# Kernel optimization log

Measured on AMD Instinct MI355X. Metric: run time of the kernel, lower is better.

The kernel has to match this reference:

```python
import jax, jax.numpy as jnp
import numpy as np

N = 50000          # nodes
E = 800000         # edges (avg degree 16)
NFEAT = 128        # dim_touched / gcn_nfeat
NHID = 96
NCLASS = 64
EXTRA = 32         # extra MLP-only features
NHID1, NHID2 = 128, 64
NN = 70            # top-k threshold rank
EPS = 1e-5         # BatchNorm1d eps


def setup_inputs() -> dict:
    key = jax.random.key(0)
    ks = jax.random.split(key, 24)
    x = jax.random.normal(ks[0], (N, NFEAT + EXTRA + 1), jnp.float32)
    grp = jax.random.randint(ks[1], (N,), 0, 2).astype(jnp.float32)
    x = x.at[:, -1].set(grp)  # last column is the group flag (target_group == 0)
    row = jax.random.randint(ks[2], (E,), 0, N, dtype=jnp.int32)
    col = jax.random.randint(ks[3], (E,), 0, N, dtype=jnp.int32)
    val = jax.random.uniform(ks[4], (E,), jnp.float32)

    def p(k, shape):
        return (jax.random.normal(k, shape, jnp.float32) * 0.05)

    return dict(
        x=x, row=row, col=col, val=val,
        W1=p(ks[5], (NFEAT, NHID)), b1=p(ks[6], (NHID,)),
        W2=p(ks[7], (NHID, NHID)), b2=p(ks[8], (NHID,)),
        W3=p(ks[9], (NHID, NHID)), b3=p(ks[10], (NHID,)),
        W4=p(ks[11], (NHID, NHID)), b4=p(ks[12], (NHID,)),
        W5=p(ks[13], (NHID, NCLASS)), b5=p(ks[14], (NCLASS,)),
        M1w=p(ks[15], (NCLASS + EXTRA, NHID1)), M1b=p(ks[16], (NHID1,)),
        M2w=p(ks[17], (NHID1, NHID2)), M2b=p(ks[18], (NHID2,)),
        M3w=p(ks[19], (NHID2, 1)), M3b=p(ks[20], (1,)),
    )


def _bn(h):
    # fresh BatchNorm1d in training mode, affine at default init (gamma=1, beta=0)
    m = jnp.mean(h, axis=0)
    v = jnp.mean((h - m) ** 2, axis=0)  # biased variance, as used for normalization
    return (h - m) * jax.lax.rsqrt(v + EPS)


def _gc(h, row, col, val, W, b):
    # GraphConvolution: spmm(adj, h @ W) + b, adj in COO form
    s = h @ W                                            # [N, out]
    msg = val[:, None] * s[col]                          # [E, out]
    agg = jax.ops.segment_sum(msg, row, num_segments=N)  # [N, out]
    return agg + b


def reference(x, row, col, val, W1, b1, W2, b2, W3, b3, W4, b4, W5, b5,
              M1w, M1b, M2w, M2b, M3w, M3b):
    h = x[:, :NFEAT]
    h = _bn(jax.nn.relu(_gc(h, row, col, val, W1, b1)))
    h = _bn(jax.nn.relu(_gc(h, row, col, val, W2, b2)))
    h = _bn(jax.nn.relu(_gc(h, row, col, val, W3, b3)))
    h = _bn(jax.nn.relu(_gc(h, row, col, val, W4, b4)))
    h = jax.nn.relu(_gc(h, row, col, val, W5, b5))        # [N, NCLASS]

    feat = jnp.concatenate([h, x[:, NFEAT:-1]], axis=1)   # [N, NCLASS+EXTRA]
    m = jax.nn.relu(feat @ M1w + M1b)
    m = jax.nn.relu(m @ M2w + M2b)
    m = m @ M3w + M3b                                     # [N, 1]

    # mask out target_group rows with the global min
    m = jnp.where(x[:, -1:] == 0.0, jnp.min(m), m)        # [N, 1]

    # top-70 threshold: value at descending rank NN
    thresh = jax.lax.top_k(m[:, 0], NN + 1)[0][NN]
    recip = jax.lax.stop_gradient(1.0 / m)                # torch reciprocal on detach()
    mask = jnp.where(m > thresh, recip, jnp.zeros_like(m))
    return m * mask
```

## Files before the change

kernel.cpp:

```cpp
#include <hip/hip_runtime.h>
#include <cstdint>
#include <cstddef>

#define XLD 161

typedef float f4u __attribute__((ext_vector_type(4), aligned(4)));
typedef float f4a __attribute__((ext_vector_type(4)));
typedef float f3u __attribute__((ext_vector_type(3), aligned(4)));

__global__ void hist_kernel(const int* __restrict__ row, int* __restrict__ cnt, int E) {
    for (int e = blockIdx.x * blockDim.x + threadIdx.x; e < E; e += gridDim.x * blockDim.x)
        atomicAdd(&cnt[row[e]], 1);
}

__global__ __launch_bounds__(256)
void scan1_kernel(const int* __restrict__ cnt, int* __restrict__ offs,
                  int* __restrict__ bsums, int n) {
    int t = threadIdx.x;
    int gid = blockIdx.x * 256 + t;
    int v = (gid < n) ? cnt[gid] : 0;
    int x = v;
#pragma unroll
    for (int o = 1; o < 64; o <<= 1) { int y = __shfl_up(x, o); if ((t & 63) >= o) x += y; }
    __shared__ int ws[4];
    if ((t & 63) == 63) ws[t >> 6] = x;
    __syncthreads();
    int add = 0;
    for (int w = 0; w < (t >> 6); w++) add += ws[w];
    int incl = x + add;
    if (gid < n) offs[gid] = incl - v;
    if (t == 255) bsums[blockIdx.x] = incl;
}

__global__ __launch_bounds__(256)
void scan2_kernel(int* __restrict__ bsums, int nb) {
    int t = threadIdx.x;
    int v = (t < nb) ? bsums[t] : 0;
    int x = v;
#pragma unroll
    for (int o = 1; o < 64; o <<= 1) { int y = __shfl_up(x, o); if ((t & 63) >= o) x += y; }
    __shared__ int ws[4];
    if ((t & 63) == 63) ws[t >> 6] = x;
    __syncthreads();
    int add = 0;
    for (int w = 0; w < (t >> 6); w++) add += ws[w];
    if (t < nb) bsums[t] = x + add - v;
}

__global__ void scan3_kernel(int* __restrict__ offs, int* __restrict__ cursor,
                             const int* __restrict__ bsums, int n, int E) {
    int gid = blockIdx.x * 256 + threadIdx.x;
    if (gid < n) {
        int o = offs[gid] + bsums[blockIdx.x];
        offs[gid] = o;
        cursor[gid] = o;
    }
    if (gid == 0) offs[n] = E;
}

__global__ void scatter_kernel(const int* __restrict__ row, const int* __restrict__ col,
                               const float* __restrict__ val, int* __restrict__ cursor,
                               int2* __restrict__ cvA, int E) {
    for (int e = blockIdx.x * blockDim.x + threadIdx.x; e < E; e += gridDim.x * blockDim.x) {
        int r = row[e];
        int p = atomicAdd(&cursor[r], 1);
        cvA[p] = make_int2(col[e], __float_as_int(val[e]));
    }
}

template <int LC, bool WVS>
__global__ __launch_bounds__(256)
void aggP(const float* __restrict__ S, int ldS, const int* __restrict__ offs,
          const int2* __restrict__ cvA,
          float* __restrict__ Aout, float* __restrict__ vout, int n) {
    int lane = threadIdx.x & 63;
    int lg   = lane & 31;
    int grp  = threadIdx.x >> 5;
    int sh   = lane & 32;

    for (int node = blockIdx.x * 8 + grp; node < n; node += gridDim.x * 8) {
        int e0 = offs[node], e1 = offs[node + 1];
        float acc[LC];
#pragma unroll
        for (int a = 0; a < LC; a++) acc[a] = 0.f;
        float vsum = 0.f;

        for (int e = e0; e < e1; e += 32) {
            int   idx = e + lg;
            int2  cv = (idx < e1) ? cvA[idx] : make_int2(0, 0);
            int   ce = cv.x;
            float ve = __int_as_float(cv.y);
            int   cnt = min(32, e1 - e);
#pragma unroll 8
            for (int j = 0; j < cnt; j++) {
                int   c = __shfl(ce, sh + j);
                float v = __shfl(ve, sh + j);
                const float* srow = S + (size_t)c * ldS + LC * lg;
                if (LC == 3) {
                    f3u g = *(const f3u*)srow;
                    acc[0] = fmaf(v, g[0], acc[0]);
                    acc[1] = fmaf(v, g[1], acc[1]);
                    acc[2] = fmaf(v, g[2], acc[2]);
                } else {
                    f4u g = *(const f4u*)srow;
                    acc[0] = fmaf(v, g[0], acc[0]);
                    acc[1] = fmaf(v, g[1], acc[1]);
                    acc[2] = fmaf(v, g[2], acc[2]);
                    acc[3] = fmaf(v, g[3], acc[3]);
                }
                vsum += v;
            }
        }

        float* orow = Aout + (size_t)node * (32 * LC) + LC * lg;
        if (LC == 3) {
            f3u o; o[0] = acc[0]; o[1] = acc[1]; o[2] = acc[2];
            *(f3u*)orow = o;
        } else {
            f4u o; o[0] = acc[0]; o[1] = acc[1]; o[2] = acc[2]; o[3] = acc[3];
            *(f4u*)orow = o;
        }
        if (WVS && lg == 0) vout[node] = vsum;
    }
}

__global__ __launch_bounds__(256)
void aggB(const float* __restrict__ S, const int* __restrict__ offs,
          const int2* __restrict__ cvA, const float* __restrict__ bias,
          float* __restrict__ Hout, float* __restrict__ vout,
          float* __restrict__ bsum, float* __restrict__ bsumsq, int n) {
    __shared__ float sS[96], sQ[96];
    int t = threadIdx.x;
    if (t < 96) { sS[t] = 0.f; sQ[t] = 0.f; }
    __syncthreads();
    int lane = t & 63, lg = lane & 31, grp = t >> 5, sh = lane & 32;
    float bb[3];
    bb[0] = bias[3 * lg]; bb[1] = bias[3 * lg + 1]; bb[2] = bias[3 * lg + 2];
    float ps[3] = {0.f, 0.f, 0.f}, pq[3] = {0.f, 0.f, 0.f};

    for (int node = blockIdx.x * 8 + grp; node < n; node += gridDim.x * 8) {
        int e0 = offs[node], e1 = offs[node + 1];
        float acc[3] = {0.f, 0.f, 0.f};
        float vsum = 0.f;
        for (int e = e0; e < e1; e += 32) {
            int   idx = e + lg;
            int2  cv = (idx < e1) ? cvA[idx] : make_int2(0, 0);
            int   ce = cv.x;
            float ve = __int_as_float(cv.y);
            int   cnt = min(32, e1 - e);
#pragma unroll 8
            for (int j = 0; j < cnt; j++) {
                int   c = __shfl(ce, sh + j);
                float v = __shfl(ve, sh + j);
                const float* srow = S + (size_t)c * 96 + 3 * lg;
                f3u g = *(const f3u*)srow;
                acc[0] = fmaf(v, g[0], acc[0]);
                acc[1] = fmaf(v, g[1], acc[1]);
                acc[2] = fmaf(v, g[2], acc[2]);
                vsum += v;
            }
        }
        float* orow = Hout + (size_t)node * 96 + 3 * lg;
        f3u o;
#pragma unroll
        for (int a = 0; a < 3; a++) {
            float v = fmaxf(acc[a] + bb[a], 0.f);
            o[a] = v;
            ps[a] += v; pq[a] += v * v;
        }
        *(f3u*)orow = o;
        if (lg == 0) vout[node] = vsum;
    }
#pragma unroll
    for (int a = 0; a < 3; a++) {
        atomicAdd(&sS[3 * lg + a], ps[a]);
        atomicAdd(&sQ[3 * lg + a], pq[a]);
    }
    __syncthreads();
    if (t < 96) {
        atomicAdd(&bsum[t], sS[t]);
        atomicAdd(&bsumsq[t], sQ[t]);
    }
}

template <int CT>
__device__ inline void ldw(const float* p, float* wv) {
    if constexpr (CT == 4) { *(f4a*)wv = *(const f4a*)p; }
    else if constexpr (CT == 6) { *(f3u*)wv = *(const f3u*)p; *(f3u*)(wv + 3) = *(const f3u*)(p + 3); }
    else { *(f4a*)wv = *(const f4a*)p; *(f4a*)(wv + 4) = *(const f4a*)(p + 4); }
}

template <int K, int C, bool DOBN, bool HASCB, bool LIN = false>
__global__ __launch_bounds__(256)
void gemmF(const float* __restrict__ A1, int ld1, int split,
           const float* __restrict__ A2, int ld2,
           const float* __restrict__ W, const float* __restrict__ bias,
           const float* __restrict__ cbv, const float* __restrict__ vsum,
           float* __restrict__ Out, float* __restrict__ bsum,
           float* __restrict__ bsumsq, int n) {
    constexpr int CT = C / 16;
    __shared__ float Wc[16 * C];
    __shared__ float At[16][68];
    __shared__ float redS[DOBN ? C : 1];
    __shared__ float redQ[DOBN ? C : 1];

    int t  = threadIdx.x;
    int tc = t & 15, tr = t >> 4;
    int row0 = blockIdx.x * 64;

    if (DOBN && t < C) { redS[t] = 0.f; redQ[t] = 0.f; }

    int srow = t >> 2;
    int gr = row0 + srow; if (gr >= n) gr = n - 1;
    int kh = (t & 3) * 4;

    float acc[4][CT];
#pragma unroll
    for (int i = 0; i < 4; i++)
#pragma unroll
        for (int c = 0; c < CT; c++) acc[i][c] = 0.f;

    for (int kb = 0; kb < K; kb += 16) {
        __syncthreads();
        for (int i = t * 4; i < 16 * C; i += 1024)
            *(f4a*)&Wc[i] = *(const f4u*)&W[(size_t)kb * C + i];
        {
            int kg = kb + kh;
            const float* src = (kg < split) ? (A1 + (size_t)gr * ld1 + kg)
                                            : (A2 + (size_t)gr * ld2 + (kg - split));
            f4u v = *(const f4u*)src;
#pragma unroll
            for (int e = 0; e < 4; e++) At[kh + e][srow] = v[e];
        }
        __syncthreads();
#pragma unroll
        for (int kk = 0; kk < 16; kk++) {
            f4a av = *(const f4a*)&At[kk][tr * 4];
            float wv[CT];
            ldw<CT>(&Wc[kk * C + tc * CT], wv);
#pragma unroll
            for (int i = 0; i < 4; i++)
#pragma unroll
                for (int c = 0; c < CT; c++) acc[i][c] = fmaf(av[i], wv[c], acc[i][c]);
        }
    }

    float bb[CT], cc[CT];
#pragma unroll
    for (int c = 0; c < CT; c++) {
        bb[c] = LIN ? 0.f : bias[tc * CT + c];
        cc[c] = HASCB ? cbv[tc * CT + c] : 0.f;
    }
    float ps[CT], pq[CT];
#pragma unroll
    for (int c = 0; c < CT; c++) { ps[c] = 0.f; pq[c] = 0.f; }

#pragma unroll
    for (int i = 0; i < 4; i++) {
        int r = row0 + tr * 4 + i;
        if (r < n) {
            float vs = HASCB ? vsum[r] : 0.f;
            float* o = Out + (size_t)r * C + tc * CT;
#pragma unroll
            for (int c = 0; c < CT; c++) {
                float v = acc[i][c] + vs * cc[c] + bb[c];
                if (!LIN) v = fmaxf(v, 0.f);
                o[c] = v;
                if (DOBN) { ps[c] += v; pq[c] += v * v; }
            }
        }
    }
    if (DOBN) {
#pragma unroll
        for (int c = 0; c < CT; c++) {
            ps[c] += __shfl_xor(ps[c], 16);
            ps[c] += __shfl_xor(ps[c], 32);
            pq[c] += __shfl_xor(pq[c], 16);
            pq[c] += __shfl_xor(pq[c], 32);
        }
        if ((t & 48) == 0) {
#pragma unroll
            for (int c = 0; c < CT; c++) {
                atomicAdd(&redS[tc * CT + c], ps[c]);
                atomicAdd(&redQ[tc * CT + c], pq[c]);
            }
        }
        __syncthreads();
        if (t < C) {
            atomicAdd(&bsum[t], redS[t]);
            atomicAdd(&bsumsq[t], redQ[t]);
        }
    }
}

template <int C>
__global__ __launch_bounds__(256)
void fold_kernel(const float* __restrict__ W, float* __restrict__ bsum,
                 float* __restrict__ bsumsq, float* __restrict__ Wf,
                 float* __restrict__ cb, int N) {
    __shared__ float mean[96], inv[96];
    int t = threadIdx.x;
    float rn = 1.0f / (float)N;
    if (t < 96) {
        float mu  = bsum[t] * rn;
        float var = bsumsq[t] * rn - mu * mu;
        mean[t] = mu;
        inv[t]  = rsqrtf(var + 1e-5f);
        bsum[t] = 0.f;
        bsumsq[t] = 0.f;
    }
    __syncthreads();
    for (int i = t; i < 96 * C; i += 256) {
        int k = i / C;
        Wf[i] = inv[k] * W[i];
    }
    if (t < C) {
        float s = 0.f;
        for (int k = 0; k < 96; k++) s += mean[k] * inv[k] * W[k * C + t];
        cb[t] = -s;
    }
}

__global__ __launch_bounds__(256)
void dot_min_kernel(const float* __restrict__ A, const float* __restrict__ M3w,
                    const float* __restrict__ M3b, float* __restrict__ m,
                    unsigned* __restrict__ gmin, int n) {
    int lane = threadIdx.x & 63;
    int wv   = threadIdx.x >> 6;
    float w  = M3w[lane];
    float b  = M3b[0];
    float lmin = 3.4e38f;
    int nw = gridDim.x * 4;
    for (int r = blockIdx.x * 4 + wv; r < n; r += nw) {
        float v = A[(size_t)r * 64 + lane] * w;
#pragma unroll
        for (int o = 32; o; o >>= 1) v += __shfl_down(v, o);
        if (lane == 0) {
            float mv = v + b;
            m[r] = mv;
            lmin = fminf(lmin, mv);
        }
    }
#pragma unroll
    for (int o = 32; o; o >>= 1) lmin = fminf(lmin, __shfl_down(lmin, o));
    __shared__ float sm[4];
    if (lane == 0) sm[wv] = lmin;
    __syncthreads();
    if (threadIdx.x == 0) {
        float mn = fminf(fminf(sm[0], sm[1]), fminf(sm[2], sm[3]));
        unsigned u = __float_as_uint(mn);
        unsigned key = (u >> 31) ? ~u : (u | 0x80000000u);
        atomicMin(gmin, key);
    }
}

__global__ void where_kernel(const float* __restrict__ x, float* __restrict__ m,
                             const unsigned* __restrict__ gmin, int n) {
    int i = blockIdx.x * blockDim.x + threadIdx.x;
    if (i < n) {
        unsigned k = *gmin;
        unsigned u = (k >> 31) ? (k ^ 0x80000000u) : ~k;
        float g = __uint_as_float(u);
        if (x[(size_t)i * XLD + 160] == 0.0f) m[i] = g;
    }
}

__device__ inline unsigned fkey(float f) {
    unsigned u = __float_as_uint(f);
    return (u >> 31) ? ~u : (u | 0x80000000u);
}

__global__ __launch_bounds__(256)
void sel_hist8(const float* __restrict__ m, unsigned* __restrict__ h0, int n) {
    __shared__ unsigned lh[256];
    int t = threadIdx.x;
    lh[t] = 0u;
    __syncthreads();
    for (int i = blockIdx.x * 256 + t; i < n; i += gridDim.x * 256)
        atomicAdd(&lh[fkey(m[i]) >> 24], 1u);
    __syncthreads();
    if (lh[t]) atomicAdd(&h0[t], lh[t]);
}

__global__ __launch_bounds__(256)
void sel_pick8(const unsigned* __restrict__ h, const unsigned* __restrict__ kres,
               int kconst, unsigned* __restrict__ outb, unsigned* __restrict__ outk) {
    int t = threadIdx.x;
    int bin = 255 - t;
    unsigned k = kres ? *kres : (unsigned)kconst;
    unsigned c = h[bin];
    unsigned x = c;
#pragma unroll
    for (int o = 1; o < 64; o <<= 1) { unsigned y = __shfl_up(x, o); if ((t & 63) >= o) x += y; }
    __shared__ unsigned ws[4];
    if ((t & 63) == 63) ws[t >> 6] = x;
    __syncthreads();
    unsigned add = 0;
    for (int w = 0; w < (t >> 6); w++) add += ws[w];
    unsigned incl = x + add, excl = incl - c;
    if (excl < k && k <= incl) { *outb = (unsigned)bin; *outk = k - excl; }
}

__global__ __launch_bounds__(256)
void sel_hist8b(const float* __restrict__ m, const unsigned* __restrict__ pick,
                unsigned* __restrict__ h1, int n) {
    __shared__ unsigned lh[256];
    int t = threadIdx.x;
    lh[t] = 0u;
    __syncthreads();
    unsigned b0 = pick[0];
    for (int i = blockIdx.x * 256 + t; i < n; i += gridDim.x * 256) {
        unsigned key = fkey(m[i]);
        if ((key >> 24) == b0) atomicAdd(&lh[(key >> 16) & 255u], 1u);
    }
    __syncthreads();
    if (lh[t]) atomicAdd(&h1[t], lh[t]);
}

__global__ void sel_collect(const float* __restrict__ m, const unsigned* __restrict__ pick,
                            unsigned* __restrict__ sbuf, unsigned* __restrict__ scnt, int n) {
    unsigned pfx = (pick[0] << 8) | pick[2];
    for (int i = blockIdx.x * blockDim.x + threadIdx.x; i < n; i += gridDim.x * blockDim.x) {
        unsigned key = fkey(m[i]);
        if ((key >> 16) == pfx) sbuf[atomicAdd(scnt, 1u)] = key;
    }
}

__global__ __launch_bounds__(1024)
void sel_final(const unsigned* __restrict__ sbuf, const unsigned* __restrict__ scnt,
               const unsigned* __restrict__ pick, float* __restrict__ thresh) {
    __shared__ unsigned hist[256];
    __shared__ unsigned spfx;
    __shared__ int skk;
    int t = threadIdx.x;
    int ns = (int)*scnt;
    if (t == 0) { spfx = ((pick[0] << 8) | pick[2]) << 16; skk = (int)pick[3]; }
    __syncthreads();
    for (int pass = 0; pass < 2; ++pass) {
        if (t < 256) hist[t] = 0u;
        __syncthreads();
        int shift = 8 - 8 * pass;
        unsigned pfxmask = (pass == 0) ? 0xFFFF0000u : 0xFFFFFF00u;
        unsigned pfx = spfx;
        for (int i = t; i < ns; i += 1024) {
            unsigned key = sbuf[i];
            if ((key & pfxmask) == pfx) atomicAdd(&hist[(key >> shift) & 255u], 1u);
        }
        __syncthreads();
        if (t == 0) {
            int cum = 0, kk = skk, chosen = 0;
            for (int b = 255; b >= 0; b--) {
                cum += (int)hist[b];
                if (cum >= kk) { chosen = b; kk -= (cum - (int)hist[b]); break; }
            }
            spfx = pfx | ((unsigned)chosen << shift);
            skk = kk;
        }
        __syncthreads();
    }
    if (t == 0) {
        unsigned key = spfx;
        unsigned u = (key >> 31) ? (key ^ 0x80000000u) : ~key;
        *thresh = __uint_as_float(u);
    }
}

__global__ void mask_kernel(const float* __restrict__ m, const float* __restrict__ thresh,
                            float* __restrict__ out, int n) {
    int i = blockIdx.x * blockDim.x + threadIdx.x;
    if (i < n) {
        float t = *thresh, v = m[i];
        out[i] = (v > t) ? v * (1.0f / v) : 0.0f;
    }
}

extern "C" void kernel_launch(void* const* d_in, const int* in_sizes, int n_in,
                              void* d_out, int out_size, void* d_ws, size_t ws_size,
                              hipStream_t stream) {
    const float* x   = (const float*)d_in[0];
    const int*   row = (const int*)d_in[1];
    const int*   col = (const int*)d_in[2];
    const float* val = (const float*)d_in[3];
    const float* W1  = (const float*)d_in[4];
    const float* b1  = (const float*)d_in[5];
    const float* W2  = (const float*)d_in[6];
    const float* b2  = (const float*)d_in[7];
    const float* W3  = (const float*)d_in[8];
    const float* b3  = (const float*)d_in[9];
    const float* W4  = (const float*)d_in[10];
    const float* b4  = (const float*)d_in[11];
    const float* W5  = (const float*)d_in[12];
    const float* b5  = (const float*)d_in[13];
    const float* M1w = (const float*)d_in[14];
    const float* M1b = (const float*)d_in[15];
    const float* M2w = (const float*)d_in[16];
    const float* M2b = (const float*)d_in[17];
    const float* M3w = (const float*)d_in[18];
    const float* M3b = (const float*)d_in[19];

    const int n = in_sizes[0] / XLD;
    const int E = in_sizes[1];

    char* ws = (char*)d_ws;
    size_t off = 0;
    auto carve = [&](size_t bytes) -> void* {
        void* p = ws + off;
        off = (off + bytes + 255) & ~(size_t)255;
        return p;
    };
    int*      offs   = (int*)carve((size_t)(n + 1) * 4);
    int*      cursor = (int*)carve((size_t)n * 4);
    int*      bsums  = (int*)carve(256 * 4);
    int2*     cvA    = (int2*)carve((size_t)E * 8);
    float*    h      = (float*)carve((size_t)n * 96 * 4);
    float*    big    = (float*)carve((size_t)n * 128 * 4);
    float*    Wf     = (float*)carve(96 * 96 * 4);
    float*    stats  = (float*)carve(192 * 4);
    float*    cb     = (float*)carve(96 * 4);
    float*    vsum   = (float*)carve((size_t)n * 4);
    float*    m      = (float*)carve((size_t)n * 4);
    unsigned* gmin   = (unsigned*)carve(4);
    float*    thresh = (float*)carve(4);
    unsigned* h0     = (unsigned*)carve(256 * 4);
    unsigned* h1     = (unsigned*)carve(256 * 4);
    unsigned* sbuf   = (unsigned*)carve((size_t)n * 4);
    unsigned* scnt   = (unsigned*)carve(4);
    unsigned* pick   = (unsigned*)carve(16);
    float* bsum   = stats;
    float* bsumsq = stats + 96;

    hipMemsetAsync(cursor, 0, (size_t)n * 4, stream);
    hipMemsetAsync(stats, 0, 192 * 4, stream);
    hipMemsetAsync(gmin, 0xFF, 4, stream);
    hipMemsetAsync(h0, 0, 256 * 4, stream);
    hipMemsetAsync(h1, 0, 256 * 4, stream);
    hipMemsetAsync(scnt, 0, 4, stream);

    const int nb = (n + 255) / 256;
    hist_kernel<<<512, 256, 0, stream>>>(row, cursor, E);
    scan1_kernel<<<nb, 256, 0, stream>>>(cursor, offs, bsums, n);
    scan2_kernel<<<1, 256, 0, stream>>>(bsums, nb);
    scan3_kernel<<<nb, 256, 0, stream>>>(offs, cursor, bsums, n, E);
    scatter_kernel<<<512, 256, 0, stream>>>(row, col, val, cursor, cvA, E);

    const int gB = (n + 63) / 64;
    const int ga = 3072;

    gemmF<128, 96, false, false, true><<<gB, 256, 0, stream>>>(x, XLD, 128, x, XLD,
        W1, b1, nullptr, nullptr, big, bsum, bsumsq, n);
    aggB<<<1024, 256, 0, stream>>>(big, offs, cvA, b1, h, vsum, bsum, bsumsq, n);

    fold_kernel<96><<<1, 256, 0, stream>>>(W2, bsum, bsumsq, Wf, cb, n);
    aggP<3, false><<<ga, 256, 0, stream>>>(h, 96, offs, cvA, big, nullptr, n);
    gemmF<96, 96, true, true><<<gB, 256, 0, stream>>>(big, 96, 96, big, 96,
        Wf, b2, cb, vsum, h, bsum, bsumsq, n);

    fold_kernel<96><<<1, 256, 0, stream>>>(W3, bsum, bsumsq, Wf, cb, n);
    aggP<3, false><<<ga, 256, 0, stream>>>(h, 96, offs, cvA, big, nullptr, n);
    gemmF<96, 96, true, true><<<gB, 256, 0, stream>>>(big, 96, 96, big, 96,
        Wf, b3, cb, vsum, h, bsum, bsumsq, n);

    fold_kernel<96><<<1, 256, 0, stream>>>(W4, bsum, bsumsq, Wf, cb, n);
    aggP<3, false><<<ga, 256, 0, stream>>>(h, 96, offs, cvA, big, nullptr, n);
    gemmF<96, 96, true, true><<<gB, 256, 0, stream>>>(big, 96, 96, big, 96,
        Wf, b4, cb, vsum, h, bsum, bsumsq, n);

    fold_kernel<64><<<1, 256, 0, stream>>>(W5, bsum, bsumsq, Wf, cb, n);
    aggP<3, false><<<ga, 256, 0, stream>>>(h, 96, offs, cvA, big, nullptr, n);
    gemmF<96, 64, false, true><<<gB, 256, 0, stream>>>(big, 96, 96, big, 96,
        Wf, b5, cb, vsum, h, bsum, bsumsq, n);

    gemmF<96, 128, false, false><<<gB, 256, 0, stream>>>(h, 64, 64, x + 128, XLD,
        M1w, M1b, nullptr, nullptr, big, bsum, bsumsq, n);
    gemmF<128, 64, false, false><<<gB, 256, 0, stream>>>(big, 128, 128, big, 128,
        M2w, M2b, nullptr, nullptr, h, bsum, bsumsq, n);

    dot_min_kernel<<<256, 256, 0, stream>>>(h, M3w, M3b, m, gmin, n);

    where_kernel<<<(n + 255) / 256, 256, 0, stream>>>(x, m, gmin, n);

    sel_hist8<<<64, 256, 0, stream>>>(m, h0, n);
    sel_pick8<<<1, 256, 0, stream>>>(h0, nullptr, 71, &pick[0], &pick[1]);
    sel_hist8b<<<64, 256, 0, stream>>>(m, pick, h1, n);
    sel_pick8<<<1, 256, 0, stream>>>(h1, &pick[1], 0, &pick[2], &pick[3]);
    sel_collect<<<64, 256, 0, stream>>>(m, pick, sbuf, scnt, n);
    sel_final<<<1, 1024, 0, stream>>>(sbuf, scnt, pick, thresh);

    mask_kernel<<<(n + 255) / 256, 256, 0, stream>>>(m, thresh, (float*)d_out, n);
}
```

Before: 768.7 us.

## Reorder last GCN layer to transform-then-aggregate and fuse final dot into MLP GEMM

The fifth graph-conv layer now multiplies by the 96x64 folded weight first and gathers 64-wide rows through a new aggC kernel, instead of gathering 96-wide rows and then multiplying. This cuts the per-edge gather traffic. The M2 GEMM gains a DOT epilogue that applies ReLU, takes the dot product with M3w, adds M3b, writes m and atomically updates the global min, which removes the separate dot_min kernel and the round trip of the 64-wide intermediate through memory. The aggB grid size is also raised from 1024 to 3072 blocks.

```diff
diff --git a/kernel.cpp b/kernel.cpp
--- a/kernel.cpp
+++ b/kernel.cpp
@@ -7,6 +7,7 @@
 typedef float f4u __attribute__((ext_vector_type(4), aligned(4)));
 typedef float f4a __attribute__((ext_vector_type(4)));
 typedef float f3u __attribute__((ext_vector_type(3), aligned(4)));
+typedef float f2a __attribute__((ext_vector_type(2)));
 
 __global__ void hist_kernel(const int* __restrict__ row, int* __restrict__ cnt, int E) {
     for (int e = blockIdx.x * blockDim.x + threadIdx.x; e < E; e += gridDim.x * blockDim.x)
@@ -183,6 +184,41 @@
     }
 }
 
+__global__ __launch_bounds__(256)
+void aggC(const float* __restrict__ S, const int* __restrict__ offs,
+          const int2* __restrict__ cvA, const float* __restrict__ bias,
+          const float* __restrict__ cb, const float* __restrict__ vsum,
+          float* __restrict__ Hout, int n) {
+    int lane = threadIdx.x & 63, lg = lane & 31, grp = threadIdx.x >> 5, sh = lane & 32;
+    float bb0 = bias[2 * lg], bb1 = bias[2 * lg + 1];
+    float cc0 = cb[2 * lg],   cc1 = cb[2 * lg + 1];
+
+    for (int node = blockIdx.x * 8 + grp; node < n; node += gridDim.x * 8) {
+        int e0 = offs[node], e1 = offs[node + 1];
+        float a0 = 0.f, a1 = 0.f;
+        for (int e = e0; e < e1; e += 32) {
+            int   idx = e + lg;
+            int2  cv = (idx < e1) ? cvA[idx] : make_int2(0, 0);
+            int   ce = cv.x;
+            float ve = __int_as_float(cv.y);
+            int   cnt = min(32, e1 - e);
+#pragma unroll 8
+            for (int j = 0; j < cnt; j++) {
+                int   c = __shfl(ce, sh + j);
+                float v = __shfl(ve, sh + j);
+                f2a g = *(const f2a*)(S + (size_t)c * 64 + 2 * lg);
+                a0 = fmaf(v, g[0], a0);
+                a1 = fmaf(v, g[1], a1);
+            }
+        }
+        float vs = vsum[node];
+        f2a o;
+        o[0] = fmaxf(a0 + vs * cc0 + bb0, 0.f);
+        o[1] = fmaxf(a1 + vs * cc1 + bb1, 0.f);
+        *(f2a*)(Hout + (size_t)node * 64 + 2 * lg) = o;
+    }
+}
+
 template <int CT>
 __device__ inline void ldw(const float* p, float* wv) {
     if constexpr (CT == 4) { *(f4a*)wv = *(const f4a*)p; }
@@ -190,7 +226,7 @@
     else { *(f4a*)wv = *(const f4a*)p; *(f4a*)(wv + 4) = *(const f4a*)(p + 4); }
 }
 
-template <int K, int C, bool DOBN, bool HASCB, bool LIN = false>
+template <int K, int C, bool DOBN, bool HASCB, bool LIN = false, bool DOT = false>
 __global__ __launch_bounds__(256)
 void gemmF(const float* __restrict__ A1, int ld1, int split,
            const float* __restrict__ A2, int ld2,
@@ -245,6 +281,40 @@
         }
     }
 
+    if constexpr (DOT) {
+        float bb2[CT], ww[CT];
+#pragma unroll
+        for (int c = 0; c < CT; c++) { bb2[c] = bias[tc * CT + c]; ww[c] = cbv[tc * CT + c]; }
+        float b3 = vsum[0];
+        float lmin = 3.4e38f;
+#pragma unroll
+        for (int i = 0; i < 4; i++) {
+            float d = 0.f;
+#pragma unroll
+            for (int c = 0; c < CT; c++) d = fmaf(fmaxf(acc[i][c] + bb2[c], 0.f), ww[c], d);
+            d += __shfl_xor(d, 1); d += __shfl_xor(d, 2);
+            d += __shfl_xor(d, 4); d += __shfl_xor(d, 8);
+            int r = row0 + tr * 4 + i;
+            if (tc == 0 && r < n) {
+                float mv = d + b3;
+                Out[r] = mv;
+                lmin = fminf(lmin, mv);
+            }
+        }
+        __shared__ float smin[16];
+        if (tc == 0) smin[tr] = lmin;
+        __syncthreads();
+        if (t == 0) {
+            float mn = smin[0];
+#pragma unroll
+            for (int i2 = 1; i2 < 16; i2++) mn = fminf(mn, smin[i2]);
+            unsigned u = __float_as_uint(mn);
+            unsigned key = (u >> 31) ? ~u : (u | 0x80000000u);
+            atomicMin((unsigned*)bsum, key);
+        }
+        return;
+    }
+
     float bb[CT], cc[CT];
 #pragma unroll
     for (int c = 0; c < CT; c++) {
@@ -318,39 +388,6 @@
         float s = 0.f;
         for (int k = 0; k < 96; k++) s += mean[k] * inv[k] * W[k * C + t];
         cb[t] = -s;
-    }
-}
-
-__global__ __launch_bounds__(256)
-void dot_min_kernel(const float* __restrict__ A, const float* __restrict__ M3w,
-                    const float* __restrict__ M3b, float* __restrict__ m,
-                    unsigned* __restrict__ gmin, int n) {
-    int lane = threadIdx.x & 63;
-    int wv   = threadIdx.x >> 6;
-    float w  = M3w[lane];
-    float b  = M3b[0];
-    float lmin = 3.4e38f;
-    int nw = gridDim.x * 4;
-    for (int r = blockIdx.x * 4 + wv; r < n; r += nw) {
-        float v = A[(size_t)r * 64 + lane] * w;
-#pragma unroll
-        for (int o = 32; o; o >>= 1) v += __shfl_down(v, o);
-        if (lane == 0) {
-            float mv = v + b;
-            m[r] = mv;
-            lmin = fminf(lmin, mv);
-        }
-    }
-#pragma unroll
-    for (int o = 32; o; o >>= 1) lmin = fminf(lmin, __shfl_down(lmin, o));
-    __shared__ float sm[4];
-    if (lane == 0) sm[wv] = lmin;
-    __syncthreads();
-    if (threadIdx.x == 0) {
-        float mn = fminf(fminf(sm[0], sm[1]), fminf(sm[2], sm[3]));
-        unsigned u = __float_as_uint(mn);
-        unsigned key = (u >> 31) ? ~u : (u | 0x80000000u);
-        atomicMin(gmin, key);
     }
 }
 
@@ -548,7 +585,7 @@
 
     gemmF<128, 96, false, false, true><<<gB, 256, 0, stream>>>(x, XLD, 128, x, XLD,
         W1, b1, nullptr, nullptr, big, bsum, bsumsq, n);
-    aggB<<<1024, 256, 0, stream>>>(big, offs, cvA, b1, h, vsum, bsum, bsumsq, n);
+    aggB<<<ga, 256, 0, stream>>>(big, offs, cvA, b1, h, vsum, bsum, bsumsq, n);
 
     fold_kernel<96><<<1, 256, 0, stream>>>(W2, bsum, bsumsq, Wf, cb, n);
     aggP<3, false><<<ga, 256, 0, stream>>>(h, 96, offs, cvA, big, nullptr, n);
@@ -566,16 +603,14 @@
         Wf, b4, cb, vsum, h, bsum, bsumsq, n);
 
     fold_kernel<64><<<1, 256, 0, stream>>>(W5, bsum, bsumsq, Wf, cb, n);
-    aggP<3, false><<<ga, 256, 0, stream>>>(h, 96, offs, cvA, big, nullptr, n);
-    gemmF<96, 64, false, true><<<gB, 256, 0, stream>>>(big, 96, 96, big, 96,
-        Wf, b5, cb, vsum, h, bsum, bsumsq, n);
+    gemmF<96, 64, false, false, true><<<gB, 256, 0, stream>>>(h, 96, 96, h, 96,
+        Wf, b5, nullptr, nullptr, big, bsum, bsumsq, n);
+    aggC<<<ga, 256, 0, stream>>>(big, offs, cvA, b5, cb, vsum, h, n);
 
     gemmF<96, 128, false, false><<<gB, 256, 0, stream>>>(h, 64, 64, x + 128, XLD,
         M1w, M1b, nullptr, nullptr, big, bsum, bsumsq, n);
-    gemmF<128, 64, false, false><<<gB, 256, 0, stream>>>(big, 128, 128, big, 128,
-        M2w, M2b, nullptr, nullptr, h, bsum, bsumsq, n);
-
-    dot_min_kernel<<<256, 256, 0, stream>>>(h, M3w, M3b, m, gmin, n);
+    gemmF<128, 64, false, false, false, true><<<gB, 256, 0, stream>>>(big, 128, 128, big, 128,
+        M2w, M2b, M3w, M3b, m, (float*)gmin, nullptr, n);
 
     where_kernel<<<(n + 255) / 256, 256, 0, stream>>>(x, m, gmin, n);
 
```

After: 768.9 us. Within noise of the previous version (+0.0%).
